# Optimization experiments

Hardware: AMD Instinct MI355X
Metric: run time of the kernel (lower is better)

## Reference

```python
import jax, jax.numpy as jnp
import numpy as np

N, DIN, DOUT, R, E = 100000, 128, 256, 4, 600000
EPS = 1e-12


def setup_inputs() -> dict:
    key = jax.random.key(0)
    ks = jax.random.split(key, 8)
    x = jax.random.normal(ks[0], (N, DIN), dtype=jnp.float32)
    edge_index = jax.random.randint(ks[1], (R, 2, E), 0, N, dtype=jnp.int32)
    s1 = 1.0 / np.sqrt(DIN)
    s2 = 1.0 / np.sqrt(DOUT)
    W1n = jax.random.uniform(ks[2], (R, DOUT, DIN), jnp.float32, -s1, s1)
    W1r = jax.random.uniform(ks[3], (R, DOUT, DIN), jnp.float32, -s1, s1)
    b1 = jnp.zeros((R, DOUT), jnp.float32)
    W2n = jax.random.uniform(ks[4], (R, DOUT, DOUT), jnp.float32, -s2, s2)
    W2r = jax.random.uniform(ks[5], (R, DOUT, DOUT), jnp.float32, -s2, s2)
    b2 = jnp.zeros((R, DOUT), jnp.float32)
    return {"x": x, "edge_index": edge_index, "W1n": W1n, "b1": b1,
            "W1r": W1r, "W2n": W2n, "b2": b2, "W2r": W2r}


def _hetero_sage_layer(x, edge_index, Wn, b, Wr):
    # per-relation sum-aggregate of source features into destinations: [R, N, D]
    agg = jax.vmap(
        lambda e: jax.ops.segment_sum(x[e[0]], e[1], num_segments=N)
    )(edge_index)
    # SAGEConv: lin_l(agg) + bias + lin_r(x); mean across relations (to_hetero aggr='mean')
    out = (jnp.einsum('rnd,rod->rno', agg, Wn)
           + b[:, None, :]
           + jnp.einsum('nd,rod->rno', x, Wr))
    return out.mean(axis=0)  # [N, DOUT]


def _l2_normalize(h):
    nrm = jnp.sqrt(jnp.sum(h * h, axis=-1, keepdims=True))
    return h / jnp.maximum(nrm, EPS)


def reference(x, edge_index, W1n, b1, W1r, W2n, b2, W2r):
    h = _hetero_sage_layer(x, edge_index, W1n, b1, W1r)
    h = jax.nn.relu(_l2_normalize(h))  # dropout is identity in eval mode
    out = _hetero_sage_layer(h, edge_index, W2n, b2, W2r)
    return out  # x_dict['note']
```

## Files before the change

### kernel.cpp

```cpp
#include <hip/hip_runtime.h>
#include <hip/hip_bf16.h>

#define NN 100000
#define DIN 128
#define DOUT 256
#define RR 4
#define EE 600000
#define NB (RR * NN)
#define SCAN_BLKS 400
#define SCAN_CHUNK 1000
#define PBLKS 2048

typedef __attribute__((ext_vector_type(4))) float f32x4;
typedef __attribute__((ext_vector_type(8))) short short8;
typedef __attribute__((ext_vector_type(2))) uint uint2v;

__device__ __forceinline__ float bf2f(ushort u) {
    union { unsigned int i; float f; } v; v.i = ((unsigned int)u) << 16; return v.f;
}
__device__ __forceinline__ ushort f2bf(float f) {
    union { float f; unsigned int i; } v; v.f = f;
    unsigned int r = v.i + 0x7fff + ((v.i >> 16) & 1);
    return (ushort)(r >> 16);
}

__device__ __forceinline__ void ld_g2l16(const void* g, void* l) {
    __builtin_amdgcn_global_load_lds(
        (const __attribute__((address_space(1))) void*)g,
        (__attribute__((address_space(3))) void*)l, 16, 0, 0);
}

__device__ __forceinline__ void store_w(ushort* W, int kd, int o, float s) {
    W[((size_t)(kd >> 6) * 256 + o) * 64 + (kd & 63)] = f2bf(s);
}

#define W1ELEMS (5 * 128 * 256)
#define W2ELEMS (5 * 256 * 256)
__global__ void wprep_all(const float* __restrict__ W1n, const float* __restrict__ W1r,
                          const float* __restrict__ W2n, const float* __restrict__ W2r,
                          const float* __restrict__ b1, const float* __restrict__ b2,
                          ushort* __restrict__ W1c, ushort* __restrict__ W2c,
                          float* __restrict__ b1s, float* __restrict__ b2s) {
    int idx = blockIdx.x * blockDim.x + threadIdx.x;
    if (idx < W1ELEMS) {
        int p = idx / (128 * 256), rem = idx - p * (128 * 256);
        int k = rem & 127, o = rem >> 7;
        float s;
        if (p == 0) {
            s = 0.f;
            for (int r = 0; r < RR; ++r) s += W1r[(size_t)r * DOUT * DIN + (long)o * DIN + k];
        } else {
            s = W1n[(size_t)(p - 1) * DOUT * DIN + (long)o * DIN + k];
        }
        store_w(W1c, p * 128 + k, o, s * 0.25f);
        return;
    }
    idx -= W1ELEMS;
    if (idx < W2ELEMS) {
        int p = idx / (256 * 256), rem = idx - p * (256 * 256);
        int k = rem & 255, o = rem >> 8;
        float s;
        if (p == 0) {
            s = 0.f;
            for (int r = 0; r < RR; ++r) s += W2r[(size_t)r * DOUT * DOUT + (long)o * DOUT + k];
        } else {
            s = W2n[(size_t)(p - 1) * DOUT * DOUT + (long)o * DOUT + k];
        }
        store_w(W2c, p * 256 + k, o, s * 0.25f);
        return;
    }
    idx -= W2ELEMS;
    if (idx < 512) {
        int o = idx & 255;
        const float* b = (idx < 256) ? b1 : b2;
        float s = 0.f;
        for (int r = 0; r < RR; ++r) s += b[(long)r * 256 + o];
        ((idx < 256) ? b1s : b2s)[o] = s * 0.25f;
    }
}

__global__ __launch_bounds__(256) void deg_count(const int* __restrict__ ei,
                                                 int* __restrict__ deg) {
    const int CH = EE / 4;
    int p = blockIdx.x & 7;
    const int stride = (PBLKS / 8) * 256;
    for (int idx = (blockIdx.x >> 3) * 256 + threadIdx.x; idx < RR * CH; idx += stride) {
        int r = idx / CH, j = idx - r * CH;
        int4 d = ((const int4*)(ei + (size_t)r * 2 * EE + EE))[j];
        if (((d.x >> 8) & 7) == p) atomicAdd(&deg[r * NN + d.x], 1);
        if (((d.y >> 8) & 7) == p) atomicAdd(&deg[r * NN + d.y], 1);
        if (((d.z >> 8) & 7) == p) atomicAdd(&deg[r * NN + d.z], 1);
        if (((d.w >> 8) & 7) == p) atomicAdd(&deg[r * NN + d.w], 1);
    }
}

__global__ __launch_bounds__(256) void fill_csr(const int* __restrict__ ei,
                                                int* __restrict__ cursor,
                                                int* __restrict__ elist) {
    const int CH = EE / 4;
    int p = blockIdx.x & 7;
    const int stride = (PBLKS / 8) * 256;
    for (int idx = (blockIdx.x >> 3) * 256 + threadIdx.x; idx < RR * CH; idx += stride) {
        int r = idx / CH, j = idx - r * CH;
        int4 d = ((const int4*)(ei + (size_t)r * 2 * EE + EE))[j];
        int4 s = ((const int4*)(ei + (size_t)r * 2 * EE))[j];
        if (((d.x >> 8) & 7) == p) elist[atomicAdd(&cursor[r * NN + d.x], 1)] = s.x;
        if (((d.y >> 8) & 7) == p) elist[atomicAdd(&cursor[r * NN + d.y], 1)] = s.y;
        if (((d.z >> 8) & 7) == p) elist[atomicAdd(&cursor[r * NN + d.z], 1)] = s.z;
        if (((d.w >> 8) & 7) == p) elist[atomicAdd(&cursor[r * NN + d.w], 1)] = s.w;
    }
}

__global__ __launch_bounds__(256) void scan_part(const int* __restrict__ deg,
                                                 int* __restrict__ bsum) {
    int b = blockIdx.x, t = threadIdx.x;
    int s = 0;
    for (int i = t; i < SCAN_CHUNK; i += 256) s += deg[b * SCAN_CHUNK + i];
    for (int o = 32; o > 0; o >>= 1) s += __shfl_down(s, o);
    __shared__ int red[4];
    if ((t & 63) == 0) red[t >> 6] = s;
    __syncthreads();
    if (t == 0) bsum[b] = red[0] + red[1] + red[2] + red[3];
}

__global__ __launch_bounds__(512) void scan_top(int* __restrict__ bsum) {
    __shared__ int v[512];
    int t = threadIdx.x;
    v[t] = (t < SCAN_BLKS) ? bsum[t] : 0;
    __syncthreads();
    for (int st = 1; st < 512; st <<= 1) {
        int tmp = (t >= st) ? v[t - st] : 0;
        __syncthreads();
        v[t] += tmp;
        __syncthreads();
    }
    if (t < SCAN_BLKS) bsum[t] = (t == 0) ? 0 : v[t - 1];
}

__global__ __launch_bounds__(256) void scan_final(int* __restrict__ degc,
                                                  const int* __restrict__ bsum,
                                                  int* __restrict__ off) {
    __shared__ int lv[1024];
    __shared__ int ts[256];
    int b = blockIdx.x, t = threadIdx.x;
    for (int i = t; i < 1024; i += 256)
        lv[i] = (i < SCAN_CHUNK) ? degc[b * SCAN_CHUNK + i] : 0;
    __syncthreads();
    int i0 = t * 4;
    int v0 = lv[i0], v1 = lv[i0 + 1], v2 = lv[i0 + 2], v3 = lv[i0 + 3];
    ts[t] = v0 + v1 + v2 + v3;
    __syncthreads();
    for (int st = 1; st < 256; st <<= 1) {
        int tmp = (t >= st) ? ts[t - st] : 0;
        __syncthreads();
        ts[t] += tmp;
        __syncthreads();
    }
    int run = bsum[b] + (t ? ts[t - 1] : 0);
    if (i0 < SCAN_CHUNK) {
        int base = b * SCAN_CHUNK + i0;
        off[base + 0] = run; degc[base + 0] = run; run += v0;
        off[base + 1] = run; degc[base + 1] = run; run += v1;
        off[base + 2] = run; degc[base + 2] = run; run += v2;
        off[base + 3] = run; degc[base + 3] = run; run += v3;
    }
    if (b == SCAN_BLKS - 1 && t == 255) off[NB] = bsum[b] + ts[255];
}

__global__ void cvt_x(const float* __restrict__ x, ushort* __restrict__ XB) {
    int t = blockIdx.x * blockDim.x + threadIdx.x;
    if (t >= NN * 32) return;
    int n = t >> 5, c4 = (t & 31) * 4;
    float4 v = *(const float4*)&x[(size_t)n * 128 + c4];
    ushort4 o = {f2bf(v.x), f2bf(v.y), f2bf(v.z), f2bf(v.w)};
    *(ushort4*)&XB[(size_t)n * 128 + c4] = o;
}

template <int D>
__global__ void gather_bf16(const ushort* __restrict__ feat,
                            const int* __restrict__ elist, const int* __restrict__ off,
                            ushort* __restrict__ agg, int sout, int chunk) {
    constexpr int V = D / 64;
    int wv = blockIdx.x * 4 + (threadIdx.x >> 6);
    int lane = threadIdx.x & 63;
    if (wv >= NN * chunk) return;
    int n = wv / chunk, rl = wv - n * chunk;
    int b = rl * NN + n;
    int beg = __builtin_amdgcn_readfirstlane(off[b]);
    int end = __builtin_amdgcn_readfirstlane(off[b + 1]);
    float acc[V];
#pragma unroll
    for (int v = 0; v < V; ++v) acc[v] = 0.f;
    const ushort* fbase = feat + lane * V;
    int e = beg;
    for (; e + 4 <= end; e += 4) {
        int s0 = elist[e], s1 = elist[e + 1], s2 = elist[e + 2], s3 = elist[e + 3];
        if constexpr (V == 2) {
            ushort2 a0 = *(const ushort2*)(fbase + (size_t)s0 * D);
            ushort2 a1 = *(const ushort2*)(fbase + (size_t)s1 * D);
            ushort2 a2 = *(const ushort2*)(fbase + (size_t)s2 * D);
            ushort2 a3 = *(const ushort2*)(fbase + (size_t)s3 * D);
            acc[0] += (bf2f(a0.x) + bf2f(a1.x)) + (bf2f(a2.x) + bf2f(a3.x));
            acc[1] += (bf2f(a0.y) + bf2f(a1.y)) + (bf2f(a2.y) + bf2f(a3.y));
        } else {
            ushort4 a0 = *(const ushort4*)(fbase + (size_t)s0 * D);
            ushort4 a1 = *(const ushort4*)(fbase + (size_t)s1 * D);
            ushort4 a2 = *(const ushort4*)(fbase + (size_t)s2 * D);
            ushort4 a3 = *(const ushort4*)(fbase + (size_t)s3 * D);
            acc[0] += (bf2f(a0.x) + bf2f(a1.x)) + (bf2f(a2.x) + bf2f(a3.x));
            acc[1] += (bf2f(a0.y) + bf2f(a1.y)) + (bf2f(a2.y) + bf2f(a3.y));
            acc[2] += (bf2f(a0.z) + bf2f(a1.z)) + (bf2f(a2.z) + bf2f(a3.z));
            acc[3] += (bf2f(a0.w) + bf2f(a1.w)) + (bf2f(a2.w) + bf2f(a3.w));
        }
    }
    for (; e < end; ++e) {
        int s0 = elist[e];
        if constexpr (V == 2) {
            ushort2 a = *(const ushort2*)(fbase + (size_t)s0 * D);
            acc[0] += bf2f(a.x); acc[1] += bf2f(a.y);
        } else {
            ushort4 a = *(const ushort4*)(fbase + (size_t)s0 * D);
            acc[0] += bf2f(a.x); acc[1] += bf2f(a.y);
            acc[2] += bf2f(a.z); acc[3] += bf2f(a.w);
        }
    }
    ushort* op = agg + (size_t)n * sout + rl * D + lane * V;
    if constexpr (V == 2) {
        uint u = (uint)f2bf(acc[0]) | ((uint)f2bf(acc[1]) << 16);
        *(uint*)op = u;
    } else {
        uint2v u;
        u.x = (uint)f2bf(acc[0]) | ((uint)f2bf(acc[1]) << 16);
        u.y = (uint)f2bf(acc[2]) | ((uint)f2bf(acc[3]) << 16);
        *(uint2v*)op = u;
    }
}

template <int MODE>
__global__ __launch_bounds__(256, 2) void gemm_fused(
    const ushort* __restrict__ F, int ldf, int K1,
    const ushort* __restrict__ G, int ldg, int K2,
    const ushort* __restrict__ W, const float* __restrict__ bias,
    void* __restrict__ Cout, int M) {
    __shared__ ushort lA[128 * 64];
    const int tid = threadIdx.x;
    const int w = tid >> 6, lane = tid & 63;
    const int row0 = blockIdx.x * 128;

    f32x4 acc[8][4];
#pragma unroll
    for (int i = 0; i < 8; ++i)
#pragma unroll
        for (int j = 0; j < 4; ++j) acc[i][j] = {0.f, 0.f, 0.f, 0.f};

    const int arow = lane >> 3;
    const int asrc = ((lane & 7) ^ arow) << 3;
    const int ldst = lane * 8;
    const ushort* aF[4]; const ushort* aG[4];
#pragma unroll
    for (int c = 0; c < 4; ++c) {
        int rg = row0 + w * 32 + c * 8 + arow;
        if (rg > M - 1) rg = M - 1;
        aF[c] = F + (size_t)rg * ldf + asrc;
        aG[c] = G + (size_t)rg * ldg + asrc;
    }
    const ushort* wfrag = W + ((size_t)(w * 64 + (lane & 15)) * 64) + (lane >> 4) * 8;
    const int nt = (K1 + K2) >> 6;

    for (int t = 0; t < nt; ++t) {
        const ushort* wb = wfrag + (size_t)t * (256 * 64);
        short8 bfr[2][4];
#pragma unroll
        for (int ks = 0; ks < 2; ++ks)
#pragma unroll
            for (int cf = 0; cf < 4; ++cf)
                bfr[ks][cf] = *(const short8*)(wb + (size_t)cf * (16 * 64) + ks * 32);
        __syncthreads();
        int kb = t << 6;
#pragma unroll
        for (int c = 0; c < 4; ++c) {
            const ushort* src = (kb < K1) ? (aF[c] + kb) : (aG[c] + (kb - K1));
            ld_g2l16(src, &lA[(w * 32 + c * 8) * 64 + ldst]);
        }
        asm volatile("s_waitcnt vmcnt(0)" ::: "memory");
        __syncthreads();
        __builtin_amdgcn_s_setprio(1);
#pragma unroll
        for (int ks = 0; ks < 2; ++ks) {
            const int co = (((ks * 4 + (lane >> 4)) ^ (lane & 7)) << 3);
            short8 af[8];
#pragma unroll
            for (int rf = 0; rf < 8; ++rf)
                af[rf] = *(const short8*)&lA[(rf * 16 + (lane & 15)) * 64 + co];
#pragma unroll
            for (int cf = 0; cf < 4; ++cf)
#pragma unroll
                for (int rf = 0; rf < 8; ++rf)
                    acc[rf][cf] = __builtin_amdgcn_mfma_f32_16x16x32_bf16(
                        af[rf], bfr[ks][cf], acc[rf][cf], 0, 0, 0);
        }
        __builtin_amdgcn_s_setprio(0);
    }

#pragma unroll
    for (int cf = 0; cf < 4; ++cf) {
        float badd = bias[w * 64 + cf * 16 + (lane & 15)];
#pragma unroll
        for (int rf = 0; rf < 8; ++rf)
#pragma unroll
            for (int m = 0; m < 4; ++m) acc[rf][cf][m] += badd;
    }

    if constexpr (MODE == 0) {
        float* Cf = (float*)Cout;
#pragma unroll
        for (int cf = 0; cf < 4; ++cf) {
            int col = w * 64 + cf * 16 + (lane & 15);
#pragma unroll
            for (int rf = 0; rf < 8; ++rf)
#pragma unroll
                for (int m = 0; m < 4; ++m) {
                    int r = row0 + rf * 16 + (lane >> 4) * 4 + m;
                    if (r < M)
                        __builtin_nontemporal_store(acc[rf][cf][m],
                                                    &Cf[(size_t)r * 256 + col]);
                }
        }
    } else {
        float* rs = (float*)lA;
        float ss[8][4];
#pragma unroll
        for (int rf = 0; rf < 8; ++rf)
#pragma unroll
            for (int m = 0; m < 4; ++m) {
                float s = 0.f;
#pragma unroll
                for (int cf = 0; cf < 4; ++cf) s += acc[rf][cf][m] * acc[rf][cf][m];
#pragma unroll
                for (int o = 1; o < 16; o <<= 1) s += __shfl_xor(s, o);
                ss[rf][m] = s;
            }
        __syncthreads();
        if ((lane & 15) == 0) {
#pragma unroll
            for (int rf = 0; rf < 8; ++rf)
#pragma unroll
                for (int m = 0; m < 4; ++m)
                    rs[w * 128 + rf * 16 + (lane >> 4) * 4 + m] = ss[rf][m];
        }
        __syncthreads();
        uint* HBw = (uint*)Cout;
#pragma unroll
        for (int rf = 0; rf < 8; ++rf)
#pragma unroll
            for (int m = 0; m < 4; ++m) {
                int tr = rf * 16 + (lane >> 4) * 4 + m;
                float tot = rs[tr] + rs[128 + tr] + rs[256 + tr] + rs[384 + tr];
                float inv = 1.0f / fmaxf(sqrtf(tot), 1e-12f);
                int r = row0 + tr;
#pragma unroll
                for (int cf = 0; cf < 4; ++cf) {
                    float v = fmaxf(acc[rf][cf][m] * inv, 0.f);
                    uint u = f2bf(v);
                    uint pu = __shfl_xor(u, 1);
                    if (!(lane & 1) && r < M)
                        HBw[(size_t)r * 128 + ((w * 64 + cf * 16 + (lane & 15)) >> 1)] =
                            u | (pu << 16);
                }
            }
    }
}

extern "C" void kernel_launch(void* const* d_in, const int* in_sizes, int n_in,
                              void* d_out, int out_size, void* d_ws, size_t ws_size,
                              hipStream_t stream) {
    const float* x   = (const float*)d_in[0];
    const int*   ei  = (const int*)d_in[1];
    const float* W1n = (const float*)d_in[2];
    const float* b1  = (const float*)d_in[3];
    const float* W1r = (const float*)d_in[4];
    const float* W2n = (const float*)d_in[5];
    const float* b2  = (const float*)d_in[6];
    const float* W2r = (const float*)d_in[7];

    ushort* HB  = (ushort*)d_ws;
    ushort* G1  = HB + (size_t)NN * 256;
    ushort* G2  = G1 + (size_t)NN * 512;
    ushort* XB  = G2;
    int* elist  = (int*)(G2 + (size_t)NN * 1024);
    int* degc   = elist + (size_t)RR * EE;
    int* off    = degc + NB;
    int* bsum   = off + NB + 1;
    ushort* W1c = (ushort*)(bsum + 512);
    ushort* W2c = W1c + 640 * 256;
    float* b1s  = (float*)(W2c + 1280 * 256);
    float* b2s  = b1s + 256;

    hipMemsetAsync(degc, 0, (size_t)NB * sizeof(int), stream);
    deg_count<<<PBLKS, 256, 0, stream>>>(ei, degc);
    scan_part<<<SCAN_BLKS, 256, 0, stream>>>(degc, bsum);
    scan_top<<<1, 512, 0, stream>>>(bsum);
    scan_final<<<SCAN_BLKS, 256, 0, stream>>>(degc, bsum, off);
    fill_csr<<<PBLKS, 256, 0, stream>>>(ei, degc, elist);

    {
        int total = W1ELEMS + W2ELEMS + 512;
        wprep_all<<<(total + 255) / 256, 256, 0, stream>>>(W1n, W1r, W2n, W2r, b1, b2,
                                                           W1c, W2c, b1s, b2s);
    }
    cvt_x<<<(NN * 32 + 255) / 256, 256, 0, stream>>>(x, XB);

    const int ggrid = (NN + 127) / 128;

    gather_bf16<128><<<NN, 256, 0, stream>>>(XB, elist, off, G1, 512, RR);
    gemm_fused<1><<<ggrid, 256, 0, stream>>>(XB, 128, 128, G1, 512, 512, W1c, b1s, HB, NN);

    gather_bf16<256><<<NN, 256, 0, stream>>>(HB, elist, off, G2, 1024, RR);
    gemm_fused<0><<<ggrid, 256, 0, stream>>>(HB, 256, 256, G2, 1024, 1024, W2c, b2s,
                                             d_out, NN);
}
```

Measured before the change: 738.9 us.

## Double-buffer A tile in LDS and prefetch W fragments in GEMM

The fused GEMM loop now uses two LDS buffers for the A tile. It issues global-to-LDS loads for the next K step, plus register loads of the next weight fragments, before running the MFMA work on the current step. This replaces the load, wait, barrier, compute sequence and is meant to hide global memory latency behind matrix math. In exchange it doubles LDS use, adds about 32 VGPRs for the prefetched B fragments, and drops the explicit vmcnt wait, so ordering of the async LDS loads rests on the barrier at the end of each iteration.

```diff
diff --git a/kernel.cpp b/kernel.cpp
--- a/kernel.cpp
+++ b/kernel.cpp
@@ -242,7 +242,7 @@
     const ushort* __restrict__ G, int ldg, int K2,
     const ushort* __restrict__ W, const float* __restrict__ bias,
     void* __restrict__ Cout, int M) {
-    __shared__ ushort lA[128 * 64];
+    __shared__ ushort lA[2][128 * 64];
     const int tid = threadIdx.x;
     const int w = tid >> 6, lane = tid & 63;
     const int row0 = blockIdx.x * 128;
@@ -267,23 +267,38 @@
     const ushort* wfrag = W + ((size_t)(w * 64 + (lane & 15)) * 64) + (lane >> 4) * 8;
     const int nt = (K1 + K2) >> 6;
 
-    for (int t = 0; t < nt; ++t) {
-        const ushort* wb = wfrag + (size_t)t * (256 * 64);
-        short8 bfr[2][4];
-#pragma unroll
-        for (int ks = 0; ks < 2; ++ks)
-#pragma unroll
-            for (int cf = 0; cf < 4; ++cf)
-                bfr[ks][cf] = *(const short8*)(wb + (size_t)cf * (16 * 64) + ks * 32);
-        __syncthreads();
+    auto stageA = [&](int t, int buf) {
         int kb = t << 6;
 #pragma unroll
         for (int c = 0; c < 4; ++c) {
             const ushort* src = (kb < K1) ? (aF[c] + kb) : (aG[c] + (kb - K1));
-            ld_g2l16(src, &lA[(w * 32 + c * 8) * 64 + ldst]);
-        }
-        asm volatile("s_waitcnt vmcnt(0)" ::: "memory");
-        __syncthreads();
+            ld_g2l16(src, &lA[buf][(w * 32 + c * 8) * 64 + ldst]);
+        }
+    };
+
+    short8 b0[2][4], b1[2][4];
+    stageA(0, 0);
+    {
+        const ushort* wb = wfrag;
+#pragma unroll
+        for (int ks = 0; ks < 2; ++ks)
+#pragma unroll
+            for (int cf = 0; cf < 4; ++cf)
+                b0[ks][cf] = *(const short8*)(wb + (size_t)cf * (16 * 64) + ks * 32);
+    }
+    __syncthreads();
+
+    int cur = 0;
+    for (int t = 0; t < nt; ++t) {
+        if (t + 1 < nt) {
+            stageA(t + 1, cur ^ 1);
+            const ushort* wb = wfrag + (size_t)(t + 1) * (256 * 64);
+#pragma unroll
+            for (int ks = 0; ks < 2; ++ks)
+#pragma unroll
+                for (int cf = 0; cf < 4; ++cf)
+                    b1[ks][cf] = *(const short8*)(wb + (size_t)cf * (16 * 64) + ks * 32);
+        }
         __builtin_amdgcn_s_setprio(1);
 #pragma unroll
         for (int ks = 0; ks < 2; ++ks) {
@@ -291,15 +306,21 @@
             short8 af[8];
 #pragma unroll
             for (int rf = 0; rf < 8; ++rf)
-                af[rf] = *(const short8*)&lA[(rf * 16 + (lane & 15)) * 64 + co];
+                af[rf] = *(const short8*)&lA[cur][(rf * 16 + (lane & 15)) * 64 + co];
 #pragma unroll
             for (int cf = 0; cf < 4; ++cf)
 #pragma unroll
                 for (int rf = 0; rf < 8; ++rf)
                     acc[rf][cf] = __builtin_amdgcn_mfma_f32_16x16x32_bf16(
-                        af[rf], bfr[ks][cf], acc[rf][cf], 0, 0, 0);
+                        af[rf], b0[ks][cf], acc[rf][cf], 0, 0, 0);
         }
         __builtin_amdgcn_s_setprio(0);
+        __syncthreads();
+#pragma unroll
+        for (int ks = 0; ks < 2; ++ks)
+#pragma unroll
+            for (int cf = 0; cf < 4; ++cf) b0[ks][cf] = b1[ks][cf];
+        cur ^= 1;
     }
 
 #pragma unroll
@@ -327,7 +348,7 @@
                 }
         }
     } else {
-        float* rs = (float*)lA;
+        float* rs = (float*)&lA[0][0];
         float ss[8][4];
 #pragma unroll
         for (int rf = 0; rf < 8; ++rf)
@@ -340,7 +361,6 @@
                 for (int o = 1; o < 16; o <<= 1) s += __shfl_xor(s, o);
                 ss[rf][m] = s;
             }
-        __syncthreads();
         if ((lane & 15) == 0) {
 #pragma unroll
             for (int rf = 0; rf < 8; ++rf)
```

Result: no change. 749.6 us (+1.5%).
